# Performance work log

Hardware: AMD Instinct MI355X
Metric: run time of the kernel (lower is better)

## Reference

```python
import jax, jax.numpy as jnp
import numpy as np

H = 128   # hidden_dim
M = 8     # mix_dim
N = 20000 # num_nodes
E = 320000

def gelu(x):
    return jax.nn.gelu(x, approximate=False)  # torch F.gelu default is exact erf

def setup_inputs() -> dict:
    key = jax.random.key(0)
    k1, k2, k3, k4 = jax.random.split(key, 4)
    X = jax.random.normal(k1, (N, H), dtype=jnp.float32)
    edge_index = jax.random.randint(k2, (2, E), 0, N, dtype=jnp.int64)
    # Linear weights, torch layout: y = x @ W.T
    W_A = jax.random.normal(k3, (H, H), dtype=jnp.float32) / np.sqrt(H)
    W_B = jax.random.normal(k4, (M, H), dtype=jnp.float32) / np.sqrt(H)
    return {"X": X, "edge_index": edge_index, "W_A": W_A, "W_B": W_B, "num_nodes": N}

def reference(X, edge_index, W_A, W_B, num_nodes):
    src, dst = edge_index[0], edge_index[1]
    X_src = X[src]                                   # (E, h) gather
    # compute_W_tar: W_B(gelu(W_A(X_src))), input_activation=False
    W_tar_edge = gelu(X_src @ W_A.T) @ W_B.T         # (E, m)
    # per-edge outer product, scatter_add over dst
    cross = jnp.einsum('eh,em->ehm', X_src, W_tar_edge)          # (E, h, m)
    agg = jax.ops.segment_sum(cross, dst, num_segments=num_nodes) # (N, h, m)
    agg = gelu(agg)
    # gather agg back to edges, contract over mix dim
    out_edge = jnp.einsum('ehm,em->eh', agg[dst], W_tar_edge)     # (E, h)
    # scatter_mean over dst
    ones = jnp.ones((dst.shape[0],), dtype=X.dtype)
    count = jax.ops.segment_sum(ones, dst, num_segments=num_nodes)
    out_sum = jax.ops.segment_sum(out_edge, dst, num_segments=num_nodes)
    out = out_sum / jnp.maximum(count, 1.0)[:, None]
    return out
```

## Files before the change

kernel.cpp:

```cpp
#include <hip/hip_runtime.h>
#include <hip/hip_bf16.h>


#define H 128
#define MDIM 8
#define CAP 64

typedef float v2f __attribute__((ext_vector_type(2)));

__device__ __forceinline__ float gelu_f(float x) {
    float u = x * (1.0f + 0.044715f * x * x);
    float t = exp2f(u * 2.3022078f);
    return x * (1.0f - __builtin_amdgcn_rcpf(1.0f + t));
}

__global__ __launch_bounds__(256) void k_prep(const float* __restrict__ X,
                                              const float* __restrict__ WA,
                                              const float* __restrict__ WB,
                                              float* __restrict__ T,
                                              int* __restrict__ cnt, int N) {
    __shared__ float Xs[32][132];
    __shared__ float Ws[64][132];
    __shared__ float WBs[8][132];
    const int t = threadIdx.x;

    for (int i = blockIdx.x * 256 + t; i < N; i += gridDim.x * 256) cnt[i] = 0;

    const int n0 = blockIdx.x * 32;

    {
        int r = t >> 5, c4 = t & 31;
        *(float4*)&WBs[r][c4 * 4] = *(const float4*)(WB + (size_t)r * H + c4 * 4);
    }
    #pragma unroll
    for (int i = 0; i < 4; ++i) {
        int idx = t + 256 * i;
        int r = idx >> 5, c4 = idx & 31;
        int gn = n0 + r;
        float4 xv = make_float4(0.f, 0.f, 0.f, 0.f);
        if (gn < N) xv = *(const float4*)(X + (size_t)gn * H + c4 * 4);
        *(float4*)&Xs[r][c4 * 4] = xv;
    }

    const int tn  = t >> 4;
    const int tjl = t & 15;

    float hreg[2][8];

    for (int p = 0; p < 2; ++p) {
        __syncthreads();
        #pragma unroll
        for (int i = 0; i < 8; ++i) {
            int idx = t + 256 * i;
            int r = idx >> 5, c4 = idx & 31;
            *(float4*)&Ws[r][c4 * 4] =
                *(const float4*)(WA + (size_t)(p * 64 + r) * H + c4 * 4);
        }
        __syncthreads();

        const int r0 = 2 * tn, r1 = r0 + 1;
        float a0[4] = {}, a1[4] = {};
        #pragma unroll 2
        for (int k = 0; k < H; k += 4) {
            float4 x0 = *(const float4*)&Xs[r0][k];
            float4 x1 = *(const float4*)&Xs[r1][k];
            #pragma unroll
            for (int jj = 0; jj < 4; ++jj) {
                float4 b = *(const float4*)&Ws[tjl + 16 * jj][k];
                a0[jj] += x0.x * b.x + x0.y * b.y + x0.z * b.z + x0.w * b.w;
                a1[jj] += x1.x * b.x + x1.y * b.y + x1.z * b.z + x1.w * b.w;
            }
        }
        #pragma unroll
        for (int jj = 0; jj < 4; ++jj) {
            hreg[0][p * 4 + jj] = gelu_f(a0[jj]);
            hreg[1][p * 4 + jj] = gelu_f(a1[jj]);
        }
    }

    __syncthreads();
    #pragma unroll
    for (int p = 0; p < 2; ++p)
        #pragma unroll
        for (int jj = 0; jj < 4; ++jj) {
            int jc = p * 64 + tjl + 16 * jj;
            Xs[2 * tn][jc]     = hreg[0][p * 4 + jj];
            Xs[2 * tn + 1][jc] = hreg[1][p * 4 + jj];
        }
    __syncthreads();

    const int n = t >> 3, m = t & 7;
    const int gn = n0 + n;
    if (gn < N) {
        float s = 0.f;
        #pragma unroll 4
        for (int qq = 0; qq < H / 4; ++qq) {
            float4 h = *(const float4*)&Xs[n][qq * 4];
            float4 w = *(const float4*)&WBs[m][qq * 4];
            s += h.x * w.x + h.y * w.y + h.z * w.z + h.w * w.w;
        }
        T[(size_t)gn * MDIM + m] = s;
    }
}

__global__ void k_fill(const int* __restrict__ ei, int* __restrict__ cnt,
                       int* __restrict__ bucket, int E) {
    int e = blockIdx.x * 256 + threadIdx.x;
    if (e < E) {
        int s = ei[e];
        int d = ei[E + e];
        int p = atomicAdd(&cnt[d], 1);
        if (p < CAP) bucket[d * CAP + p] = s;
    }
}

__device__ __forceinline__ void fma8v(v2f* acc, v2f xv, float4 ta, float4 tb) {
    acc[0] += xv * ta.x;
    acc[1] += xv * ta.y;
    acc[2] += xv * ta.z;
    acc[3] += xv * ta.w;
    acc[4] += xv * tb.x;
    acc[5] += xv * tb.y;
    acc[6] += xv * tb.z;
    acc[7] += xv * tb.w;
}

__global__ __launch_bounds__(256) void k_main(const float* __restrict__ X,
                                              const float* __restrict__ T,
                                              const int* __restrict__ cnt,
                                              const int* __restrict__ bucket,
                                              float* __restrict__ out, int N) {
    __shared__ __attribute__((aligned(16))) int srcs[4][CAP];
    __shared__ float Tl[4][CAP][MDIM];
    const int w    = threadIdx.x >> 6;
    const int lane = threadIdx.x & 63;
    const int d    = blockIdx.x * 4 + w;
    if (d >= N) return;

    const int c  = cnt[d];
    const int cc = (c < CAP) ? c : CAP;

    if (lane < cc) {
        int s = bucket[d * CAP + lane];
        srcs[w][lane] = s;
        const float4* t4 = (const float4*)(T + (size_t)s * MDIM);
        *(float4*)&Tl[w][lane][0] = t4[0];
        *(float4*)&Tl[w][lane][4] = t4[1];
    }

    float sp = 0.f;
    {
        const int m = lane & 7, g = lane >> 3;
        for (int j = g; j < cc; j += 8) sp += Tl[w][j][m];
        sp += __shfl_xor(sp, 8);
        sp += __shfl_xor(sp, 16);
        sp += __shfl_xor(sp, 32);
    }
    float S[MDIM];
    #pragma unroll
    for (int m = 0; m < MDIM; ++m) S[m] = __shfl(sp, m);

    v2f acc[MDIM] = {};
    const float* Xl = X + 2 * lane;

    int j = 0;
    for (; j + 4 <= cc; j += 4) {
        int4 s4 = *(const int4*)&srcs[w][j];
        v2f x0 = *(const v2f*)(Xl + (size_t)s4.x * H);
        v2f x1 = *(const v2f*)(Xl + (size_t)s4.y * H);
        v2f x2 = *(const v2f*)(Xl + (size_t)s4.z * H);
        v2f x3 = *(const v2f*)(Xl + (size_t)s4.w * H);
        float4 ta0 = *(const float4*)&Tl[w][j + 0][0];
        float4 tb0 = *(const float4*)&Tl[w][j + 0][4];
        float4 ta1 = *(const float4*)&Tl[w][j + 1][0];
        float4 tb1 = *(const float4*)&Tl[w][j + 1][4];
        float4 ta2 = *(const float4*)&Tl[w][j + 2][0];
        float4 tb2 = *(const float4*)&Tl[w][j + 2][4];
        float4 ta3 = *(const float4*)&Tl[w][j + 3][0];
        float4 tb3 = *(const float4*)&Tl[w][j + 3][4];
        fma8v(acc, x0, ta0, tb0);
        fma8v(acc, x1, ta1, tb1);
        fma8v(acc, x2, ta2, tb2);
        fma8v(acc, x3, ta3, tb3);
    }
    for (; j < cc; ++j) {
        int s = srcs[w][j];
        v2f xv = *(const v2f*)(Xl + (size_t)s * H);
        float4 ta = *(const float4*)&Tl[w][j][0];
        float4 tb = *(const float4*)&Tl[w][j][4];
        fma8v(acc, xv, ta, tb);
    }

    v2f r = {0.f, 0.f};
    if (c > 0) {
        float inv = __builtin_amdgcn_rcpf((float)c);
        #pragma unroll
        for (int m = 0; m < MDIM; ++m) {
            r.x += gelu_f(acc[m].x) * S[m];
            r.y += gelu_f(acc[m].y) * S[m];
        }
        r.x *= inv;
        r.y *= inv;
    }
    *(v2f*)(out + (size_t)d * H + 2 * lane) = r;
}

extern "C" void kernel_launch(void* const* d_in, const int* in_sizes, int n_in,
                              void* d_out, int out_size, void* d_ws, size_t ws_size,
                              hipStream_t stream) {
    const float* X  = (const float*)d_in[0];
    const int*   ei = (const int*)d_in[1];
    const float* WA = (const float*)d_in[2];
    const float* WB = (const float*)d_in[3];
    float* out = (float*)d_out;

    const int N = in_sizes[0] / H;
    const int E = in_sizes[1] / 2;

    char* wp = (char*)d_ws;
    float* T    = (float*)wp;  wp += (size_t)N * MDIM * sizeof(float);
    int*   cnt  = (int*)wp;    wp += (size_t)((N + 3) & ~3) * sizeof(int);
    int*   bucket = (int*)wp;

    k_prep<<<dim3((N + 31) / 32), dim3(256), 0, stream>>>(X, WA, WB, T, cnt, N);
    k_fill<<<dim3((E + 255) / 256), dim3(256), 0, stream>>>(ei, cnt, bucket, E);
    k_main<<<dim3((N + 3) / 4), dim3(256), 0, stream>>>(X, T, cnt, bucket, out, N);
}
```

Measured before the change: 142.9 us.

## Fuse prep and bucket-fill kernels, read WA directly, deepen gather unroll

Merges the per-node T computation and the edge bucketing into one launch with block-index dispatch, moving the cnt zeroing to a memset so the two independent phases can run concurrently. The prep phase now reads WA straight from global memory, relying on cache, instead of staging it in shared memory, which removes two barriers and a large LDS buffer. The main gather loop is unrolled to 8 edges so more X loads are in flight at once. The trade-offs are higher register pressure and uncoalesced, repeated WA global reads in the prep GEMM.

```diff
diff --git a/kernel.cpp b/kernel.cpp
--- a/kernel.cpp
+++ b/kernel.cpp
@@ -14,17 +14,29 @@
     return x * (1.0f - __builtin_amdgcn_rcpf(1.0f + t));
 }
 
-__global__ __launch_bounds__(256) void k_prep(const float* __restrict__ X,
-                                              const float* __restrict__ WA,
-                                              const float* __restrict__ WB,
-                                              float* __restrict__ T,
-                                              int* __restrict__ cnt, int N) {
+__global__ __launch_bounds__(256) void k_prep_fill(const float* __restrict__ X,
+                                                   const float* __restrict__ WA,
+                                                   const float* __restrict__ WB,
+                                                   const int* __restrict__ ei,
+                                                   float* __restrict__ T,
+                                                   int* __restrict__ cnt,
+                                                   int* __restrict__ bucket,
+                                                   int N, int E, int prepBlocks) {
+    const int t = threadIdx.x;
+
+    if (blockIdx.x >= prepBlocks) {
+        int e = (blockIdx.x - prepBlocks) * 256 + t;
+        if (e < E) {
+            int s = ei[e];
+            int d = ei[E + e];
+            int p = atomicAdd(&cnt[d], 1);
+            if (p < CAP) bucket[d * CAP + p] = s;
+        }
+        return;
+    }
+
     __shared__ float Xs[32][132];
-    __shared__ float Ws[64][132];
     __shared__ float WBs[8][132];
-    const int t = threadIdx.x;
-
-    for (int i = blockIdx.x * 256 + t; i < N; i += gridDim.x * 256) cnt[i] = 0;
 
     const int n0 = blockIdx.x * 32;
 
@@ -41,24 +53,16 @@
         if (gn < N) xv = *(const float4*)(X + (size_t)gn * H + c4 * 4);
         *(float4*)&Xs[r][c4 * 4] = xv;
     }
+    __syncthreads();
 
     const int tn  = t >> 4;
     const int tjl = t & 15;
+    const int r0 = 2 * tn, r1 = r0 + 1;
 
     float hreg[2][8];
 
     for (int p = 0; p < 2; ++p) {
-        __syncthreads();
-        #pragma unroll
-        for (int i = 0; i < 8; ++i) {
-            int idx = t + 256 * i;
-            int r = idx >> 5, c4 = idx & 31;
-            *(float4*)&Ws[r][c4 * 4] =
-                *(const float4*)(WA + (size_t)(p * 64 + r) * H + c4 * 4);
-        }
-        __syncthreads();
-
-        const int r0 = 2 * tn, r1 = r0 + 1;
+        const float* w0 = WA + (size_t)(p * 64 + tjl) * H;
         float a0[4] = {}, a1[4] = {};
         #pragma unroll 2
         for (int k = 0; k < H; k += 4) {
@@ -66,7 +70,7 @@
             float4 x1 = *(const float4*)&Xs[r1][k];
             #pragma unroll
             for (int jj = 0; jj < 4; ++jj) {
-                float4 b = *(const float4*)&Ws[tjl + 16 * jj][k];
+                float4 b = *(const float4*)(w0 + (size_t)(16 * jj) * H + k);
                 a0[jj] += x0.x * b.x + x0.y * b.y + x0.z * b.z + x0.w * b.w;
                 a1[jj] += x1.x * b.x + x1.y * b.y + x1.z * b.z + x1.w * b.w;
             }
@@ -84,8 +88,8 @@
         #pragma unroll
         for (int jj = 0; jj < 4; ++jj) {
             int jc = p * 64 + tjl + 16 * jj;
-            Xs[2 * tn][jc]     = hreg[0][p * 4 + jj];
-            Xs[2 * tn + 1][jc] = hreg[1][p * 4 + jj];
+            Xs[r0][jc] = hreg[0][p * 4 + jj];
+            Xs[r1][jc] = hreg[1][p * 4 + jj];
         }
     __syncthreads();
 
@@ -100,17 +104,6 @@
             s += h.x * w.x + h.y * w.y + h.z * w.z + h.w * w.w;
         }
         T[(size_t)gn * MDIM + m] = s;
-    }
-}
-
-__global__ void k_fill(const int* __restrict__ ei, int* __restrict__ cnt,
-                       int* __restrict__ bucket, int E) {
-    int e = blockIdx.x * 256 + threadIdx.x;
-    if (e < E) {
-        int s = ei[e];
-        int d = ei[E + e];
-        int p = atomicAdd(&cnt[d], 1);
-        if (p < CAP) bucket[d * CAP + p] = s;
     }
 }
 
@@ -164,24 +157,36 @@
     const float* Xl = X + 2 * lane;
 
     int j = 0;
+    for (; j + 8 <= cc; j += 8) {
+        int4 sa = *(const int4*)&srcs[w][j];
+        int4 sb = *(const int4*)&srcs[w][j + 4];
+        v2f x0 = *(const v2f*)(Xl + (size_t)sa.x * H);
+        v2f x1 = *(const v2f*)(Xl + (size_t)sa.y * H);
+        v2f x2 = *(const v2f*)(Xl + (size_t)sa.z * H);
+        v2f x3 = *(const v2f*)(Xl + (size_t)sa.w * H);
+        v2f x4 = *(const v2f*)(Xl + (size_t)sb.x * H);
+        v2f x5 = *(const v2f*)(Xl + (size_t)sb.y * H);
+        v2f x6 = *(const v2f*)(Xl + (size_t)sb.z * H);
+        v2f x7 = *(const v2f*)(Xl + (size_t)sb.w * H);
+        #pragma unroll
+        for (int q = 0; q < 8; ++q) {
+            float4 ta = *(const float4*)&Tl[w][j + q][0];
+            float4 tb = *(const float4*)&Tl[w][j + q][4];
+            v2f xv = (q == 0) ? x0 : (q == 1) ? x1 : (q == 2) ? x2 : (q == 3) ? x3
+                   : (q == 4) ? x4 : (q == 5) ? x5 : (q == 6) ? x6 : x7;
+            fma8v(acc, xv, ta, tb);
+        }
+    }
     for (; j + 4 <= cc; j += 4) {
         int4 s4 = *(const int4*)&srcs[w][j];
         v2f x0 = *(const v2f*)(Xl + (size_t)s4.x * H);
         v2f x1 = *(const v2f*)(Xl + (size_t)s4.y * H);
         v2f x2 = *(const v2f*)(Xl + (size_t)s4.z * H);
         v2f x3 = *(const v2f*)(Xl + (size_t)s4.w * H);
-        float4 ta0 = *(const float4*)&Tl[w][j + 0][0];
-        float4 tb0 = *(const float4*)&Tl[w][j + 0][4];
-        float4 ta1 = *(const float4*)&Tl[w][j + 1][0];
-        float4 tb1 = *(const float4*)&Tl[w][j + 1][4];
-        float4 ta2 = *(const float4*)&Tl[w][j + 2][0];
-        float4 tb2 = *(const float4*)&Tl[w][j + 2][4];
-        float4 ta3 = *(const float4*)&Tl[w][j + 3][0];
-        float4 tb3 = *(const float4*)&Tl[w][j + 3][4];
-        fma8v(acc, x0, ta0, tb0);
-        fma8v(acc, x1, ta1, tb1);
-        fma8v(acc, x2, ta2, tb2);
-        fma8v(acc, x3, ta3, tb3);
+        fma8v(acc, x0, *(const float4*)&Tl[w][j + 0][0], *(const float4*)&Tl[w][j + 0][4]);
+        fma8v(acc, x1, *(const float4*)&Tl[w][j + 1][0], *(const float4*)&Tl[w][j + 1][4]);
+        fma8v(acc, x2, *(const float4*)&Tl[w][j + 2][0], *(const float4*)&Tl[w][j + 2][4]);
+        fma8v(acc, x3, *(const float4*)&Tl[w][j + 3][0], *(const float4*)&Tl[w][j + 3][4]);
     }
     for (; j < cc; ++j) {
         int s = srcs[w][j];
@@ -222,7 +227,11 @@
     int*   cnt  = (int*)wp;    wp += (size_t)((N + 3) & ~3) * sizeof(int);
     int*   bucket = (int*)wp;
 
-    k_prep<<<dim3((N + 31) / 32), dim3(256), 0, stream>>>(X, WA, WB, T, cnt, N);
-    k_fill<<<dim3((E + 255) / 256), dim3(256), 0, stream>>>(ei, cnt, bucket, E);
+    const int prepBlocks = (N + 31) / 32;
+    const int fillBlocks = (E + 255) / 256;
+
+    hipMemsetAsync(cnt, 0, (size_t)N * sizeof(int), stream);
+    k_prep_fill<<<dim3(prepBlocks + fillBlocks), dim3(256), 0, stream>>>(
+        X, WA, WB, ei, T, cnt, bucket, N, E, prepBlocks);
     k_main<<<dim3((N + 3) / 4), dim3(256), 0, stream>>>(X, T, cnt, bucket, out, N);
 }
```

Measured after the change: 189.8 us. 32.9% more time.
